# Optimization experiments

Hardware: AMD Instinct MI355X
Metric: run time of the kernel (lower is better)

## Reference

```python
import jax, jax.numpy as jnp
import numpy as np

NUM_HEADS = 4
GROUPS = 8
EPS = 1e-5


def group_norm(x, w, b):
    B, C, H, W, D = x.shape
    xg = x.reshape(B, GROUPS, C // GROUPS, H, W, D)
    mu = xg.mean(axis=(2, 3, 4, 5), keepdims=True)
    var = xg.var(axis=(2, 3, 4, 5), keepdims=True)
    xn = ((xg - mu) * jax.lax.rsqrt(var + EPS)).reshape(B, C, H, W, D)
    return xn * w[None, :, None, None, None] + b[None, :, None, None, None]


def avg_pool2x(t, H, W, D):
    # t: [N, d, H, W, D] -> [N, d, H/2, W/2, D/2] via 2x2x2 block mean
    N, d = t.shape[:2]
    t = t.reshape(N, d, H // 2, 2, W // 2, 2, D // 2, 2)
    return t.mean(axis=(3, 5, 7))


def setup_inputs() -> dict:
    key = jax.random.key(0)
    ks = jax.random.split(key, 4)
    B, C, H, W, D = 2, 128, 24, 24, 24
    x = jax.random.normal(ks[0], (B, C, H, W, D), dtype=jnp.float32)
    gn_w = jnp.ones((C,), jnp.float32)
    gn_b = jnp.zeros((C,), jnp.float32)
    qkv_w = jax.random.normal(ks[1], (3 * C, C), dtype=jnp.float32) * 0.02
    qkv_b = jnp.zeros((3 * C,), jnp.float32)
    proj_w = jax.random.normal(ks[2], (C, C), dtype=jnp.float32) * 0.02
    proj_b = jnp.zeros((C,), jnp.float32)
    return {"x": x, "gn_w": gn_w, "gn_b": gn_b, "qkv_w": qkv_w,
            "qkv_b": qkv_b, "proj_w": proj_w, "proj_b": proj_b}


def reference(x, gn_w, gn_b, qkv_w, qkv_b, proj_w, proj_b):
    B, C, H, W, D = x.shape
    hd = C // NUM_HEADS
    spatial = H * W * D
    residual = x

    xn = group_norm(x, gn_w, gn_b)
    # 1x1x1 conv == channel matmul
    qkv = jnp.einsum('oc,bchwd->bohwd', qkv_w, xn) + qkv_b[None, :, None, None, None]
    qkv = qkv.reshape(B, 3, NUM_HEADS, hd, spatial)
    q, k, v = qkv[:, 0], qkv[:, 1], qkv[:, 2]  # [B, h, d, N]

    if spatial > 1024:
        k3 = k.reshape(B * NUM_HEADS, hd, H, W, D)
        v3 = v.reshape(B * NUM_HEADS, hd, H, W, D)
        k = avg_pool2x(k3, H, W, D).reshape(B, NUM_HEADS, hd, -1)
        v = avg_pool2x(v3, H, W, D).reshape(B, NUM_HEADS, hd, -1)

    scale = hd ** -0.5
    attn = jnp.einsum('bhdn,bhdm->bhnm', q * scale, k)
    attn = jax.nn.softmax(attn, axis=-1)
    out = jnp.einsum('bhnm,bhdm->bhdn', attn, v)
    out = out.reshape(B, C, H, W, D)
    out = jnp.einsum('oc,bchwd->bohwd', proj_w, out) + proj_b[None, :, None, None, None]
    return out + residual
```

## Files before the change

kernel.cpp:

```cpp
#include <hip/hip_runtime.h>
#include <hip/hip_bf16.h>

#define SB 2
#define SC 128
#define SS 13824
#define SNH 4
#define SHD 32
#define SKV 1728
#define GN_N 221184.0f
#define QSCALE 0.25504771249f

typedef unsigned int uint;
typedef unsigned short ushort;
typedef __bf16 bf16x8 __attribute__((ext_vector_type(8)));
typedef float f32x16 __attribute__((ext_vector_type(16)));

__device__ inline ushort f2bf(float v){
  __hip_bfloat16 h = __float2bfloat16(v);
  return *reinterpret_cast<ushort*>(&h);
}
__device__ inline float bf2f(ushort u){
  union { ushort s[2]; float f; } x; x.s[0] = 0; x.s[1] = u; return x.f;
}
__device__ inline uint pk2(float a, float b){
  __hip_bfloat162 h = __float22bfloat162_rn(make_float2(a, b));
  return *reinterpret_cast<uint*>(&h);
}
__device__ inline bf16x8 ldg8(const ushort* p){
  union { uint4 q; bf16x8 b; } u;
  u.q = *reinterpret_cast<const uint4*>(p);
  return u.b;
}
__device__ inline f32x16 mfma32(bf16x8 a, bf16x8 b, f32x16 c){
  return __builtin_amdgcn_mfma_f32_32x32x16_bf16(a, b, c, 0, 0, 0);
}
__device__ inline int rowmap(int r, int hl){
  return (r & 3) + 8 * ((r >> 2) & 1) + 4 * hl + 16 * (r >> 3);
}
__device__ inline float vexp2(float x){
  float r;
  asm("v_exp_f32 %0, %1" : "=v"(r) : "v"(x));
  return r;
}

__global__ __launch_bounds__(256) void k_stats(const float* __restrict__ x, float* __restrict__ chsums){
  int bid = blockIdx.x;
  int b = bid >> 7, c = bid & 127;
  const float4* p = reinterpret_cast<const float4*>(x + (size_t)(b * 128 + c) * SS);
  float s = 0.f, q = 0.f;
  for (int i = threadIdx.x; i < SS / 4; i += 256){
    float4 v = p[i];
    s += v.x + v.y + v.z + v.w;
    q += v.x * v.x + v.y * v.y + v.z * v.z + v.w * v.w;
  }
  for (int off = 32; off; off >>= 1){ s += __shfl_down(s, off, 64); q += __shfl_down(q, off, 64); }
  __shared__ float ls[4][2];
  int w = threadIdx.x >> 6, lane = threadIdx.x & 63;
  if (lane == 0){ ls[w][0] = s; ls[w][1] = q; }
  __syncthreads();
  if (threadIdx.x == 0){
    float S = ls[0][0] + ls[1][0] + ls[2][0] + ls[3][0];
    float Q = ls[0][1] + ls[1][1] + ls[2][1] + ls[3][1];
    chsums[(b * 128 + c) * 2] = S;
    chsums[(b * 128 + c) * 2 + 1] = Q;
  }
}

__global__ __launch_bounds__(256) void k_params(const float* __restrict__ chsums,
                                                const float* __restrict__ gn_w, const float* __restrict__ gn_b,
                                                const float* __restrict__ qkv_w, const float* __restrict__ qkv_b,
                                                const float* __restrict__ proj_w,
                                                ushort* __restrict__ Wp, float* __restrict__ biasP,
                                                ushort* __restrict__ pw){
  int tid = blockIdx.x * 256 + threadIdx.x;
  if (tid < 768){
    int b = tid / 384, o = tid % 384;
    float mul = (o < 128) ? QSCALE : 1.0f;
    ushort* wrow = Wp + (size_t)(b * 384 + o) * 128;
    float acc = 0.f;
    for (int g = 0; g < 8; ++g){
      float S = 0.f, Q = 0.f;
      for (int ch = g * 16; ch < g * 16 + 16; ++ch){
        S += chsums[(b * 128 + ch) * 2];
        Q += chsums[(b * 128 + ch) * 2 + 1];
      }
      float mu = S * (1.0f / GN_N);
      float var = Q * (1.0f / GN_N) - mu * mu;
      float rs = rsqrtf(var + 1e-5f);
      for (int ci = 0; ci < 16; ++ci){
        int c = g * 16 + ci;
        float a = gn_w[c] * rs;
        float be = gn_b[c] - mu * a;
        float wv = qkv_w[o * 128 + c];
        acc += wv * be;
        wrow[c] = f2bf(wv * a * mul);
      }
    }
    biasP[b * 384 + o] = (qkv_b[o] + acc) * mul;
  } else if (tid < 896){
    int o = tid - 768;
    for (int c = 0; c < 128; ++c) pw[o * 128 + c] = f2bf(proj_w[o * 128 + c]);
  }
}

__global__ __launch_bounds__(128) void k_qkv(const float* __restrict__ x, const ushort* __restrict__ Wp,
                                             const float* __restrict__ biasP,
                                             ushort* __restrict__ Qt, ushort* __restrict__ KVt){
  int bid = blockIdx.x;
  int st2 = bid % 432;
  int b  = bid / 432;
  int t = threadIdx.x, w = t >> 6, lane = t & 63, hl = lane >> 5, ln = lane & 31;
  int s0 = st2 * 32;
  int s = s0 + ln;
  const float* xb = x + (size_t)b * 128 * SS;
  bf16x8 afr[8];
  #pragma unroll
  for (int ks = 0; ks < 8; ++ks){
    int cb = ks * 16 + hl * 8;
    union { ushort us[8]; bf16x8 b8; } f;
    #pragma unroll
    for (int j = 0; j < 8; ++j)
      f.us[j] = f2bf(xb[(size_t)(cb + j) * SS + s]);
    afr[ks] = f.b8;
  }
  for (int oi = 0; oi < 6; ++oi){
    int o0 = (w * 6 + oi) * 32;
    f32x16 acc = {};
    const ushort* wrow = Wp + (size_t)(b * 384 + o0 + ln) * 128 + hl * 8;
    #pragma unroll
    for (int ks = 0; ks < 8; ++ks)
      acc = mfma32(afr[ks], ldg8(wrow + ks * 16), acc);
    float bo = biasP[b * 384 + o0 + ln];
    if (o0 < 128){
      #pragma unroll
      for (int r = 0; r < 16; ++r){
        int srow = s0 + rowmap(r, hl);
        Qt[(size_t)(b * SS + srow) * 128 + o0 + ln] = f2bf(acc[r] + bo);
      }
    } else {
      #pragma unroll
      for (int r = 0; r < 16; ++r){
        int srow = s0 + rowmap(r, hl);
        KVt[(size_t)(b * SS + srow) * 256 + (o0 - 128) + ln] = f2bf(acc[r] + bo);
      }
    }
  }
}

__global__ __launch_bounds__(256) void k_pool(const ushort* __restrict__ KVt,
                                              ushort* __restrict__ kfr, ushort* __restrict__ vfr){
  int bid = blockIdx.x;
  int mt = bid % 27;
  int h  = (bid / 27) & 3;
  int b  = bid / 108;
  int m0 = mt * 64;
  int t = threadIdx.x;
  int kl = t & 63, o = t >> 6;
  int m = m0 + kl;
  int h2 = m / 144; int rem = m - h2 * 144; int w2 = rem / 12; int d2 = rem - w2 * 12;
  int sb = h2 * 1152 + w2 * 48 + d2 * 2;
  const ushort* base = KVt + (size_t)b * SS * 256 + h * 32 + o * 8;
  float ks[8] = {0,0,0,0,0,0,0,0}, vs[8] = {0,0,0,0,0,0,0,0};
  #pragma unroll
  for (int i = 0; i < 2; ++i)
    #pragma unroll
    for (int jj = 0; jj < 2; ++jj)
      #pragma unroll
      for (int kk = 0; kk < 2; ++kk){
        const ushort* row = base + (size_t)(sb + i * 576 + jj * 24 + kk) * 256;
        union { uint4 q; ushort us[8]; } K8, V8;
        K8.q = *reinterpret_cast<const uint4*>(row);
        V8.q = *reinterpret_cast<const uint4*>(row + 128);
        #pragma unroll
        for (int j = 0; j < 8; ++j){ ks[j] += bf2f(K8.us[j]); vs[j] += bf2f(V8.us[j]); }
      }
  union { uint4 q; ushort us[8]; } KW;
  #pragma unroll
  for (int j = 0; j < 8; ++j) KW.us[j] = f2bf(ks[j] * 0.125f);
  int call = 2 * (kl >> 5) + (o >> 1);
  int lane = (kl & 31) + 32 * (o & 1);
  size_t kb_ = ((size_t)((b * 4 + h) * 27 + mt) * 4 + call) * 512 + lane * 8;
  *reinterpret_cast<uint4*>(&kfr[kb_]) = KW.q;
  __shared__ ushort V_lds[32][72];
  #pragma unroll
  for (int j = 0; j < 8; ++j) V_lds[o * 8 + j][kl] = f2bf(vs[j] * 0.125f);
  __syncthreads();
  int d = t & 31, ko = t >> 5;
  uint4 vv = *reinterpret_cast<const uint4*>(&V_lds[d][ko * 8]);
  int c = ko >> 1, hl2 = ko & 1;
  int lane2 = d + 32 * hl2;
  size_t vb_ = ((size_t)((b * 4 + h) * 27 + mt) * 4 + c) * 512 + lane2 * 8;
  *reinterpret_cast<uint4*>(&vfr[vb_]) = vv;
}

#define PVSTEP(Parr, i4, vf, oac)                                    \
  {                                                                  \
    uint a0 = Parr[(i4) + 0], a1 = Parr[(i4) + 1];                   \
    uint b0 = Parr[(i4) + 2], b1 = Parr[(i4) + 3];                   \
    asm("v_permlane32_swap_b32 %0, %1" : "+v"(a0), "+v"(b0));        \
    asm("v_permlane32_swap_b32 %0, %1" : "+v"(a1), "+v"(b1));        \
    union { uint u[4]; bf16x8 b8; } pf;                              \
    pf.u[0] = a0; pf.u[1] = a1; pf.u[2] = b0; pf.u[3] = b1;          \
    oac = mfma32(vf, pf.b8, oac);                                    \
    lacc = mfma32(ones, pf.b8, lacc);                                \
  }

__global__ __launch_bounds__(128, 2) void k_attn(const ushort* __restrict__ Qt, const ushort* __restrict__ kfr,
                                                 const ushort* __restrict__ vfr, ushort* __restrict__ Ofr){
  int bid = blockIdx.x;
  int st = bid % 216;
  int bh = bid / 216;
  int h = bh & 3, b = bh >> 2;
  int t = threadIdx.x, w = t >> 6, lane = t & 63, hl = lane >> 5, ln = lane & 31;
  int n = st * 64 + w * 32 + ln;
  const ushort* qb = Qt + (size_t)(b * SS + n) * 128 + h * 32;
  bf16x8 qf0 = ldg8(qb + hl * 8);
  bf16x8 qf1 = ldg8(qb + 16 + hl * 8);
  const ushort* kbase = kfr + (size_t)bh * 27 * 2048 + (size_t)lane * 8;
  const ushort* vbase = vfr + (size_t)bh * 27 * 2048 + (size_t)lane * 8;
  union { ushort us[8]; bf16x8 b8; } one8;
  #pragma unroll
  for (int j = 0; j < 8; ++j) one8.us[j] = 0x3F80;
  bf16x8 ones = one8.b8;
  f32x16 oA = {}, oB = {}, lacc = {};
  bf16x8 kc0 = ldg8(kbase), kc1 = ldg8(kbase + 512);
  bf16x8 kc2 = ldg8(kbase + 1024), kc3 = ldg8(kbase + 1536);
  for (int it = 0; it < 27; ++it){
    const ushort* vp = vbase + it * 2048;
    bf16x8 v0 = ldg8(vp), v1 = ldg8(vp + 512), v2 = ldg8(vp + 1024), v3 = ldg8(vp + 1536);
    int itn = it + 1; if (itn == 27) itn = 0;
    const ushort* kpn = kbase + itn * 2048;
    bf16x8 kn0 = ldg8(kpn), kn1 = ldg8(kpn + 512);
    bf16x8 kn2 = ldg8(kpn + 1024), kn3 = ldg8(kpn + 1536);
    f32x16 s0 = {}, s1 = {};
    s0 = mfma32(kc0, qf0, s0);
    s0 = mfma32(kc1, qf1, s0);
    s1 = mfma32(kc2, qf0, s1);
    s1 = mfma32(kc3, qf1, s1);
    #pragma unroll
    for (int r = 0; r < 16; ++r) s0[r] = vexp2(s0[r]);
    #pragma unroll
    for (int r = 0; r < 16; ++r) s1[r] = vexp2(s1[r]);
    uint P0[8], P1[8];
    #pragma unroll
    for (int i = 0; i < 8; ++i) P0[i] = pk2(s0[2 * i], s0[2 * i + 1]);
    #pragma unroll
    for (int i = 0; i < 8; ++i) P1[i] = pk2(s1[2 * i], s1[2 * i + 1]);
    PVSTEP(P0, 0, v0, oA)
    PVSTEP(P0, 4, v1, oB)
    PVSTEP(P1, 0, v2, oA)
    PVSTEP(P1, 4, v3, oB)
    kc0 = kn0; kc1 = kn1; kc2 = kn2; kc3 = kn3;
  }
  float inv = 1.f / lacc[0];
  __shared__ ushort T[2][32 * 40];
  ushort* Tw = T[w];
  #pragma unroll
  for (int r = 0; r < 16; ++r){
    int d = rowmap(r, hl);
    Tw[ln * 40 + d] = f2bf((oA[r] + oB[r]) * inv);
  }
  __syncthreads();
  int stile = st * 2 + w;
  #pragma unroll
  for (int it2 = 0; it2 < 2; ++it2){
    int d0 = hl * 8 + it2 * 16;
    uint4 vv = *reinterpret_cast<const uint4*>(&Tw[ln * 40 + d0]);
    size_t off = ((size_t)b * 3456 + (size_t)(stile * 8 + 2 * h + it2)) * 512 + (size_t)lane * 8;
    *reinterpret_cast<uint4*>(&Ofr[off]) = vv;
  }
}

__global__ __launch_bounds__(128) void k_proj(const ushort* __restrict__ Ofr, const ushort* __restrict__ pw,
                                              const float* __restrict__ pb, const float* __restrict__ xres,
                                              float* __restrict__ out){
  int bid = blockIdx.x;
  int st32 = bid % 432;
  int b = bid / 432;
  int t = threadIdx.x, w = t >> 6, lane = t & 63, hl = lane >> 5, ln = lane & 31;
  int s = st32 * 32 + ln;
  bf16x8 bfr[8];
  #pragma unroll
  for (int ks = 0; ks < 8; ++ks){
    size_t off = ((size_t)b * 3456 + (size_t)(st32 * 8 + ks)) * 512 + (size_t)lane * 8;
    bfr[ks] = ldg8(&Ofr[off]);
  }
  for (int oi = 0; oi < 2; ++oi){
    int ot = w * 2 + oi;
    f32x16 acc = {};
    const ushort* arow = pw + (size_t)(ot * 32 + ln) * 128 + hl * 8;
    #pragma unroll
    for (int ks = 0; ks < 8; ++ks)
      acc = mfma32(ldg8(arow + ks * 16), bfr[ks], acc);
    #pragma unroll
    for (int r = 0; r < 16; ++r){
      int o = ot * 32 + rowmap(r, hl);
      size_t idx = (size_t)(b * 128 + o) * SS + s;
      out[idx] = acc[r] + pb[o] + xres[idx];
    }
  }
}

extern "C" void kernel_launch(void* const* d_in, const int* in_sizes, int n_in,
                              void* d_out, int out_size, void* d_ws, size_t ws_size,
                              hipStream_t stream){
  const float* x      = (const float*)d_in[0];
  const float* gn_w   = (const float*)d_in[1];
  const float* gn_b   = (const float*)d_in[2];
  const float* qkv_w  = (const float*)d_in[3];
  const float* qkv_b  = (const float*)d_in[4];
  const float* proj_w = (const float*)d_in[5];
  const float* proj_b = (const float*)d_in[6];
  float* out = (float*)d_out;
  char* ws = (char*)d_ws;

  float*  chsums = (float*) (ws + 0);
  ushort* Wp     = (ushort*)(ws + 2048);
  float*  biasP  = (float*) (ws + 198656);
  ushort* pw     = (ushort*)(ws + 201728);
  ushort* Qt     = (ushort*)(ws + 234496);
  ushort* KVt    = (ushort*)(ws + 7312384);
  ushort* Ofr    = (ushort*)(ws + 7312384);
  ushort* kfr    = (ushort*)(ws + 21468160);
  ushort* vfr    = (ushort*)(ws + 22352896);

  k_stats <<<256,  256, 0, stream>>>(x, chsums);
  k_params<<<4,    256, 0, stream>>>(chsums, gn_w, gn_b, qkv_w, qkv_b, proj_w, Wp, biasP, pw);
  k_qkv   <<<864,  128, 0, stream>>>(x, Wp, biasP, Qt, KVt);
  k_pool  <<<216,  256, 0, stream>>>(KVt, kfr, vfr);
  k_attn  <<<1728, 128, 0, stream>>>(Qt, kfr, vfr, Ofr);
  k_proj  <<<864,  128, 0, stream>>>(Ofr, pw, proj_b, x, out);
}
```

Before: 106.9 us.

## Fuse output projection and residual into attention kernel, pack bf16 conversions

The attention kernel now processes 32 query positions per block, with one wave per head. It writes the normalized per-head outputs into a shared tile and then applies the 128x128 projection, bias and residual add directly, so the separate projection kernel and the intermediate Ofr buffer round trip are gone. Several float-to-bf16 conversions in the qkv, pool and attention kernels now use a paired pack instead of scalar converts. In exchange, the block grows to 256 threads with a shared tile and a block-wide sync. The projection weights are re-read per block, and attention register pressure may rise from the extra accumulator and fragments.

```diff
diff --git a/kernel.cpp b/kernel.cpp
--- a/kernel.cpp
+++ b/kernel.cpp
@@ -117,10 +117,13 @@
   #pragma unroll
   for (int ks = 0; ks < 8; ++ks){
     int cb = ks * 16 + hl * 8;
-    union { ushort us[8]; bf16x8 b8; } f;
+    float xv[8];
     #pragma unroll
     for (int j = 0; j < 8; ++j)
-      f.us[j] = f2bf(xb[(size_t)(cb + j) * SS + s]);
+      xv[j] = xb[(size_t)(cb + j) * SS + s];
+    union { uint u[4]; bf16x8 b8; } f;
+    #pragma unroll
+    for (int j2 = 0; j2 < 4; ++j2) f.u[j2] = pk2(xv[2 * j2], xv[2 * j2 + 1]);
     afr[ks] = f.b8;
   }
   for (int oi = 0; oi < 6; ++oi){
@@ -133,15 +136,19 @@
     float bo = biasP[b * 384 + o0 + ln];
     if (o0 < 128){
       #pragma unroll
-      for (int r = 0; r < 16; ++r){
+      for (int r = 0; r < 16; r += 2){
         int srow = s0 + rowmap(r, hl);
-        Qt[(size_t)(b * SS + srow) * 128 + o0 + ln] = f2bf(acc[r] + bo);
+        uint pr = pk2(acc[r] + bo, acc[r + 1] + bo);
+        Qt[(size_t)(b * SS + srow) * 128 + o0 + ln] = (ushort)pr;
+        Qt[(size_t)(b * SS + srow + 1) * 128 + o0 + ln] = (ushort)(pr >> 16);
       }
     } else {
       #pragma unroll
-      for (int r = 0; r < 16; ++r){
+      for (int r = 0; r < 16; r += 2){
         int srow = s0 + rowmap(r, hl);
-        KVt[(size_t)(b * SS + srow) * 256 + (o0 - 128) + ln] = f2bf(acc[r] + bo);
+        uint pr = pk2(acc[r] + bo, acc[r + 1] + bo);
+        KVt[(size_t)(b * SS + srow) * 256 + (o0 - 128) + ln] = (ushort)pr;
+        KVt[(size_t)(b * SS + srow + 1) * 256 + (o0 - 128) + ln] = (ushort)(pr >> 16);
       }
     }
   }
@@ -174,16 +181,21 @@
         #pragma unroll
         for (int j = 0; j < 8; ++j){ ks[j] += bf2f(K8.us[j]); vs[j] += bf2f(V8.us[j]); }
       }
-  union { uint4 q; ushort us[8]; } KW;
-  #pragma unroll
-  for (int j = 0; j < 8; ++j) KW.us[j] = f2bf(ks[j] * 0.125f);
+  union { uint u[4]; uint4 q; } KW;
+  #pragma unroll
+  for (int j2 = 0; j2 < 4; ++j2)
+    KW.u[j2] = pk2(ks[2 * j2] * 0.125f, ks[2 * j2 + 1] * 0.125f);
   int call = 2 * (kl >> 5) + (o >> 1);
   int lane = (kl & 31) + 32 * (o & 1);
   size_t kb_ = ((size_t)((b * 4 + h) * 27 + mt) * 4 + call) * 512 + lane * 8;
   *reinterpret_cast<uint4*>(&kfr[kb_]) = KW.q;
   __shared__ ushort V_lds[32][72];
   #pragma unroll
-  for (int j = 0; j < 8; ++j) V_lds[o * 8 + j][kl] = f2bf(vs[j] * 0.125f);
+  for (int j2 = 0; j2 < 4; ++j2){
+    uint pv = pk2(vs[2 * j2] * 0.125f, vs[2 * j2 + 1] * 0.125f);
+    V_lds[o * 8 + 2 * j2][kl] = (ushort)pv;
+    V_lds[o * 8 + 2 * j2 + 1][kl] = (ushort)(pv >> 16);
+  }
   __syncthreads();
   int d = t & 31, ko = t >> 5;
   uint4 vv = *reinterpret_cast<const uint4*>(&V_lds[d][ko * 8]);
@@ -205,24 +217,28 @@
     lacc = mfma32(ones, pf.b8, lacc);                                \
   }
 
-__global__ __launch_bounds__(128, 2) void k_attn(const ushort* __restrict__ Qt, const ushort* __restrict__ kfr,
-                                                 const ushort* __restrict__ vfr, ushort* __restrict__ Ofr){
+__global__ __launch_bounds__(256, 2) void k_attn(const ushort* __restrict__ Qt, const ushort* __restrict__ kfr,
+                                                 const ushort* __restrict__ vfr, const ushort* __restrict__ pw,
+                                                 const float* __restrict__ pb, const float* __restrict__ xres,
+                                                 float* __restrict__ out){
   int bid = blockIdx.x;
-  int st = bid % 216;
-  int bh = bid / 216;
-  int h = bh & 3, b = bh >> 2;
+  int qt = bid % 432;
+  int b  = bid / 432;
   int t = threadIdx.x, w = t >> 6, lane = t & 63, hl = lane >> 5, ln = lane & 31;
-  int n = st * 64 + w * 32 + ln;
-  const ushort* qb = Qt + (size_t)(b * SS + n) * 128 + h * 32;
-  bf16x8 qf0 = ldg8(qb + hl * 8);
-  bf16x8 qf1 = ldg8(qb + 16 + hl * 8);
+  int n = qt * 32 + ln;
+  int h = w;
+  int bh = b * 4 + h;
+  const ushort* qrow = Qt + (size_t)(b * SS + n) * 128 + h * 32;
+  bf16x8 qf0 = ldg8(qrow + hl * 8);
+  bf16x8 qf1 = ldg8(qrow + 16 + hl * 8);
   const ushort* kbase = kfr + (size_t)bh * 27 * 2048 + (size_t)lane * 8;
   const ushort* vbase = vfr + (size_t)bh * 27 * 2048 + (size_t)lane * 8;
   union { ushort us[8]; bf16x8 b8; } one8;
   #pragma unroll
   for (int j = 0; j < 8; ++j) one8.us[j] = 0x3F80;
   bf16x8 ones = one8.b8;
-  f32x16 oA = {}, oB = {}, lacc = {};
+  const f32x16 fz = {};
+  f32x16 oA = fz, oB = fz, lacc = fz;
   bf16x8 kc0 = ldg8(kbase), kc1 = ldg8(kbase + 512);
   bf16x8 kc2 = ldg8(kbase + 1024), kc3 = ldg8(kbase + 1536);
   for (int it = 0; it < 27; ++it){
@@ -232,10 +248,9 @@
     const ushort* kpn = kbase + itn * 2048;
     bf16x8 kn0 = ldg8(kpn), kn1 = ldg8(kpn + 512);
     bf16x8 kn2 = ldg8(kpn + 1024), kn3 = ldg8(kpn + 1536);
-    f32x16 s0 = {}, s1 = {};
-    s0 = mfma32(kc0, qf0, s0);
+    f32x16 s0 = mfma32(kc0, qf0, fz);
     s0 = mfma32(kc1, qf1, s0);
-    s1 = mfma32(kc2, qf0, s1);
+    f32x16 s1 = mfma32(kc2, qf0, fz);
     s1 = mfma32(kc3, qf1, s1);
     #pragma unroll
     for (int r = 0; r < 16; ++r) s0[r] = vexp2(s0[r]);
@@ -253,51 +268,28 @@
     kc0 = kn0; kc1 = kn1; kc2 = kn2; kc3 = kn3;
   }
   float inv = 1.f / lacc[0];
-  __shared__ ushort T[2][32 * 40];
-  ushort* Tw = T[w];
+  __shared__ ushort OT[32][136];
+  #pragma unroll
+  for (int r = 0; r < 16; r += 2){
+    int d = rowmap(r, hl);
+    uint pr = pk2((oA[r] + oB[r]) * inv, (oA[r + 1] + oB[r + 1]) * inv);
+    *reinterpret_cast<uint*>(&OT[ln][h * 32 + d]) = pr;
+  }
+  __syncthreads();
+  bf16x8 bfr[8];
+  #pragma unroll
+  for (int ks = 0; ks < 8; ++ks)
+    bfr[ks] = ldg8(&OT[ln][ks * 16 + hl * 8]);
+  f32x16 acc = fz;
+  const ushort* arow = pw + (size_t)(w * 32 + ln) * 128 + hl * 8;
+  #pragma unroll
+  for (int ks = 0; ks < 8; ++ks)
+    acc = mfma32(ldg8(arow + ks * 16), bfr[ks], acc);
   #pragma unroll
   for (int r = 0; r < 16; ++r){
-    int d = rowmap(r, hl);
-    Tw[ln * 40 + d] = f2bf((oA[r] + oB[r]) * inv);
-  }
-  __syncthreads();
-  int stile = st * 2 + w;
-  #pragma unroll
-  for (int it2 = 0; it2 < 2; ++it2){
-    int d0 = hl * 8 + it2 * 16;
-    uint4 vv = *reinterpret_cast<const uint4*>(&Tw[ln * 40 + d0]);
-    size_t off = ((size_t)b * 3456 + (size_t)(stile * 8 + 2 * h + it2)) * 512 + (size_t)lane * 8;
-    *reinterpret_cast<uint4*>(&Ofr[off]) = vv;
-  }
-}
-
-__global__ __launch_bounds__(128) void k_proj(const ushort* __restrict__ Ofr, const ushort* __restrict__ pw,
-                                              const float* __restrict__ pb, const float* __restrict__ xres,
-                                              float* __restrict__ out){
-  int bid = blockIdx.x;
-  int st32 = bid % 432;
-  int b = bid / 432;
-  int t = threadIdx.x, w = t >> 6, lane = t & 63, hl = lane >> 5, ln = lane & 31;
-  int s = st32 * 32 + ln;
-  bf16x8 bfr[8];
-  #pragma unroll
-  for (int ks = 0; ks < 8; ++ks){
-    size_t off = ((size_t)b * 3456 + (size_t)(st32 * 8 + ks)) * 512 + (size_t)lane * 8;
-    bfr[ks] = ldg8(&Ofr[off]);
-  }
-  for (int oi = 0; oi < 2; ++oi){
-    int ot = w * 2 + oi;
-    f32x16 acc = {};
-    const ushort* arow = pw + (size_t)(ot * 32 + ln) * 128 + hl * 8;
-    #pragma unroll
-    for (int ks = 0; ks < 8; ++ks)
-      acc = mfma32(ldg8(arow + ks * 16), bfr[ks], acc);
-    #pragma unroll
-    for (int r = 0; r < 16; ++r){
-      int o = ot * 32 + rowmap(r, hl);
-      size_t idx = (size_t)(b * 128 + o) * SS + s;
-      out[idx] = acc[r] + pb[o] + xres[idx];
-    }
+    int o = w * 32 + rowmap(r, hl);
+    size_t idx = (size_t)(b * 128 + o) * SS + n;
+    out[idx] = acc[r] + pb[o] + xres[idx];
   }
 }
 
@@ -320,14 +312,12 @@
   ushort* pw     = (ushort*)(ws + 201728);
   ushort* Qt     = (ushort*)(ws + 234496);
   ushort* KVt    = (ushort*)(ws + 7312384);
-  ushort* Ofr    = (ushort*)(ws + 7312384);
   ushort* kfr    = (ushort*)(ws + 21468160);
   ushort* vfr    = (ushort*)(ws + 22352896);
 
-  k_stats <<<256,  256, 0, stream>>>(x, chsums);
-  k_params<<<4,    256, 0, stream>>>(chsums, gn_w, gn_b, qkv_w, qkv_b, proj_w, Wp, biasP, pw);
-  k_qkv   <<<864,  128, 0, stream>>>(x, Wp, biasP, Qt, KVt);
-  k_pool  <<<216,  256, 0, stream>>>(KVt, kfr, vfr);
-  k_attn  <<<1728, 128, 0, stream>>>(Qt, kfr, vfr, Ofr);
-  k_proj  <<<864,  128, 0, stream>>>(Ofr, pw, proj_b, x, out);
-}
+  k_stats <<<256, 256, 0, stream>>>(x, chsums);
+  k_params<<<4,   256, 0, stream>>>(chsums, gn_w, gn_b, qkv_w, qkv_b, proj_w, Wp, biasP, pw);
+  k_qkv   <<<864, 128, 0, stream>>>(x, Wp, biasP, Qt, KVt);
+  k_pool  <<<216, 256, 0, stream>>>(KVt, kfr, vfr);
+  k_attn  <<<864, 256, 0, stream>>>(Qt, kfr, vfr, pw, proj_b, x, out);
+}
```

Result: faster. 95.37 us (-10.8%).
